# Optimization experiments

Hardware: AMD Instinct MI355X
Metric: run time of the kernel (lower is better)

## Reference

```python
import jax, jax.numpy as jnp
import numpy as np


def setup_inputs() -> dict:
    key = jax.random.key(0)
    k1, k2 = jax.random.split(key)
    B, S, N, D = 4, 8, 2048, 3
    pred_points = jax.random.normal(k1, (B, S, N, D), dtype=jnp.float32)
    target_points = jax.random.normal(k2, (B, S, N, D), dtype=jnp.float32)
    return {"pred_points": pred_points, "target_points": target_points}


def reference(pred_points, target_points):
    # pred_points, target_points: [B, S, N, 3]
    seq_len = pred_points.shape[1]
    # Pairwise Euclidean distances via the GEMM identity |p-t|^2 = |p|^2 + |t|^2 - 2 p.t
    p2 = jnp.sum(pred_points * pred_points, axis=-1)      # [B,S,N]
    t2 = jnp.sum(target_points * target_points, axis=-1)  # [B,S,M]
    cross = jnp.einsum('bsnd,bsmd->bsnm', pred_points, target_points)  # [B,S,N,M]
    d2 = p2[..., :, None] + t2[..., None, :] - 2.0 * cross
    d = jnp.sqrt(jnp.maximum(d2, 0.0))  # [B,S,N,M]
    # Bidirectional nearest-neighbor min + mean over points
    min_p2t = jnp.min(d, axis=3)  # [B,S,N]
    min_t2p = jnp.min(d, axis=2)  # [B,S,M]
    chamfer = jnp.mean(min_p2t, axis=2) + jnp.mean(min_t2p, axis=2)  # [B,S]
    total_loss = jnp.sum(chamfer, axis=1)  # [B] (sum over timesteps)
    # reduction == 'mean'
    return jnp.mean(total_loss) / seq_len
```

## Files before the change

### kernel.cpp

```cpp
#include <hip/hip_runtime.h>
#include <math.h>

#define N_PTS   2048
#define BLOCK   256
#define NQ      8
#define SLAB    128
#define NSLAB   (N_PTS / SLAB)

__global__ __launch_bounds__(BLOCK) void chamfer_min_kernel(
    const float* __restrict__ pred,
    const float* __restrict__ tgt,
    unsigned int* __restrict__ wsmin)
{
    __shared__ float4 sh[SLAB];

    const int bs   = blockIdx.x;
    const int dir  = blockIdx.y;
    const int slab = blockIdx.z;
    const int tid  = threadIdx.x;

    const float* Abase = (dir ? tgt : pred) + (size_t)bs * N_PTS * 3;
    const float* Bbase = (dir ? pred : tgt) + (size_t)bs * N_PTS * 3;

    if (tid < SLAB) {
        const int j = slab * SLAB + tid;
        const float x = Bbase[3 * j + 0];
        const float y = Bbase[3 * j + 1];
        const float z = Bbase[3 * j + 2];
        sh[tid] = make_float4(x, y, z, x * x + y * y + z * z);
    }
    __syncthreads();

    float nx[NQ], ny[NQ], nz[NQ], p2[NQ], best[NQ];
    #pragma unroll
    for (int k = 0; k < NQ; ++k) {
        const int q = tid + BLOCK * k;
        const float px = Abase[3 * q + 0];
        const float py = Abase[3 * q + 1];
        const float pz = Abase[3 * q + 2];
        nx[k] = -2.0f * px;
        ny[k] = -2.0f * py;
        nz[k] = -2.0f * pz;
        p2[k] = px * px + py * py + pz * pz;
        best[k] = 3.4e38f;
    }

    #pragma unroll 2
    for (int j = 0; j < SLAB; ++j) {
        const float4 t = sh[j];
        #pragma unroll
        for (int k = 0; k < NQ; ++k) {
            const float v = fmaf(nx[k], t.x,
                            fmaf(ny[k], t.y,
                            fmaf(nz[k], t.z, t.w)));
            best[k] = fminf(best[k], v);
        }
    }

    const int base = (dir * 32 + bs) * N_PTS;
    #pragma unroll
    for (int k = 0; k < NQ; ++k) {
        const float d2 = fmaxf(p2[k] + best[k], 0.0f);
        atomicMin(&wsmin[base + tid + BLOCK * k], __float_as_uint(d2));
    }
}

__global__ __launch_bounds__(BLOCK) void chamfer_finalize_kernel(
    const float4* __restrict__ wsmin,
    float* __restrict__ out)
{
    __shared__ float red[BLOCK / 64];
    const int i = blockIdx.x * BLOCK + threadIdx.x;
    const float4 t = wsmin[i];
    float s = sqrtf(t.x) + sqrtf(t.y) + sqrtf(t.z) + sqrtf(t.w);

    for (int off = 32; off > 0; off >>= 1)
        s += __shfl_down(s, off, 64);
    const int tid = threadIdx.x;
    if ((tid & 63) == 0) red[tid >> 6] = s;
    __syncthreads();
    if (tid == 0) {
        const float blk = red[0] + red[1] + red[2] + red[3];
        atomicAdd(out, blk * (1.0f / 65536.0f));
    }
}

extern "C" void kernel_launch(void* const* d_in, const int* in_sizes, int n_in,
                              void* d_out, int out_size, void* d_ws, size_t ws_size,
                              hipStream_t stream) {
    const float* pred = (const float*)d_in[0];
    const float* tgt  = (const float*)d_in[1];
    float* out = (float*)d_out;
    unsigned int* wsmin = (unsigned int*)d_ws;

    hipMemsetAsync(wsmin, 0x7F, (size_t)131072 * sizeof(unsigned int), stream);
    hipMemsetAsync(out, 0, sizeof(float), stream);

    dim3 grid(32, 2, NSLAB);
    chamfer_min_kernel<<<grid, BLOCK, 0, stream>>>(pred, tgt, wsmin);

    chamfer_finalize_kernel<<<131072 / (BLOCK * 4), BLOCK, 0, stream>>>(
        (const float4*)wsmin, out);
}
```

Before: 81.86 us.

## Replace atomicMin workspace with per-slab partial minima reduced in finalize

Each slab block now writes its partial squared-distance minima to its own workspace slice instead of using atomicMin into a shared buffer. That removes the large memset and the atomic contention. The finalize kernel takes the min over the 16 slabs per point, clamps, takes sqrt and reduces. The inner loop is also unrolled over two target points so the fmin chains become shallower. The cost is a 16x larger workspace write and read, and finalize runs with more blocks.

```diff
diff --git a/kernel.cpp b/kernel.cpp
--- a/kernel.cpp
+++ b/kernel.cpp
@@ -10,7 +10,7 @@
 __global__ __launch_bounds__(BLOCK) void chamfer_min_kernel(
     const float* __restrict__ pred,
     const float* __restrict__ tgt,
-    unsigned int* __restrict__ wsmin)
+    float* __restrict__ ws)
 {
     __shared__ float4 sh[SLAB];
 
@@ -46,38 +46,47 @@
     }
 
     #pragma unroll 2
-    for (int j = 0; j < SLAB; ++j) {
-        const float4 t = sh[j];
+    for (int j = 0; j < SLAB; j += 2) {
+        const float4 t0 = sh[j];
+        const float4 t1 = sh[j + 1];
         #pragma unroll
         for (int k = 0; k < NQ; ++k) {
-            const float v = fmaf(nx[k], t.x,
-                            fmaf(ny[k], t.y,
-                            fmaf(nz[k], t.z, t.w)));
-            best[k] = fminf(best[k], v);
+            const float v0 = fmaf(nx[k], t0.x,
+                             fmaf(ny[k], t0.y,
+                             fmaf(nz[k], t0.z, t0.w)));
+            const float v1 = fmaf(nx[k], t1.x,
+                             fmaf(ny[k], t1.y,
+                             fmaf(nz[k], t1.z, t1.w)));
+            best[k] = fminf(best[k], fminf(v0, v1));
         }
     }
 
-    const int base = (dir * 32 + bs) * N_PTS;
+    float* dst = ws + ((size_t)(dir * NSLAB + slab) * 32 + bs) * N_PTS;
     #pragma unroll
-    for (int k = 0; k < NQ; ++k) {
-        const float d2 = fmaxf(p2[k] + best[k], 0.0f);
-        atomicMin(&wsmin[base + tid + BLOCK * k], __float_as_uint(d2));
-    }
+    for (int k = 0; k < NQ; ++k)
+        dst[tid + BLOCK * k] = p2[k] + best[k];
 }
 
 __global__ __launch_bounds__(BLOCK) void chamfer_finalize_kernel(
-    const float4* __restrict__ wsmin,
+    const float* __restrict__ ws,
     float* __restrict__ out)
 {
     __shared__ float red[BLOCK / 64];
     const int i = blockIdx.x * BLOCK + threadIdx.x;
-    const float4 t = wsmin[i];
-    float s = sqrtf(t.x) + sqrtf(t.y) + sqrtf(t.z) + sqrtf(t.w);
+    const int dir = i >> 16;
+    const int bsq = i & 0xFFFF;
+
+    float m = 3.4e38f;
+    #pragma unroll
+    for (int s = 0; s < NSLAB; ++s) {
+        m = fminf(m, ws[(size_t)(dir * NSLAB + s) * 65536 + bsq]);
+    }
+    float d = sqrtf(fmaxf(m, 0.0f));
 
     for (int off = 32; off > 0; off >>= 1)
-        s += __shfl_down(s, off, 64);
+        d += __shfl_down(d, off, 64);
     const int tid = threadIdx.x;
-    if ((tid & 63) == 0) red[tid >> 6] = s;
+    if ((tid & 63) == 0) red[tid >> 6] = d;
     __syncthreads();
     if (tid == 0) {
         const float blk = red[0] + red[1] + red[2] + red[3];
@@ -91,14 +100,12 @@
     const float* pred = (const float*)d_in[0];
     const float* tgt  = (const float*)d_in[1];
     float* out = (float*)d_out;
-    unsigned int* wsmin = (unsigned int*)d_ws;
+    float* ws = (float*)d_ws;
 
-    hipMemsetAsync(wsmin, 0x7F, (size_t)131072 * sizeof(unsigned int), stream);
     hipMemsetAsync(out, 0, sizeof(float), stream);
 
     dim3 grid(32, 2, NSLAB);
-    chamfer_min_kernel<<<grid, BLOCK, 0, stream>>>(pred, tgt, wsmin);
+    chamfer_min_kernel<<<grid, BLOCK, 0, stream>>>(pred, tgt, ws);
 
-    chamfer_finalize_kernel<<<131072 / (BLOCK * 4), BLOCK, 0, stream>>>(
-        (const float4*)wsmin, out);
+    chamfer_finalize_kernel<<<131072 / BLOCK, BLOCK, 0, stream>>>(ws, out);
 }
```

Result: slower. 87.06 us (+6.3%).
